# Kernel optimization log

Measured on AMD Instinct MI355X. Metric: run time of the kernel, lower is better.

Reference implementation:

```python
import jax, jax.numpy as jnp
import numpy as np

N_NODES = 50000
N_EDGES = 600000
IN_C, HID_C, OUT_C = 128, 128, 64
NUM_GRAPHS = 512


def sage_conv(x, src, dst, Wl, bl, Wr):
    """PyG SAGEConv (aggr='mean'): out = mean_{j->i} x_j @ Wl + bl + x_i @ Wr."""
    n = x.shape[0]
    msg = x[src]  # [E, d] gather
    agg = jax.ops.segment_sum(msg, dst, num_segments=n)
    deg = jax.ops.segment_sum(jnp.ones((src.shape[0], 1), x.dtype), dst, num_segments=n)
    agg = agg / jnp.maximum(deg, 1.0)
    return agg @ Wl + bl + x @ Wr


def setup_inputs() -> dict:
    key = jax.random.key(0)
    ks = jax.random.split(key, 12)
    x = jax.random.normal(ks[0], (N_NODES, IN_C), dtype=jnp.float32)
    edge_index = jax.random.randint(ks[1], (2, N_EDGES), 0, N_NODES, dtype=jnp.int32)
    cluster = jnp.sort(jax.random.randint(ks[2], (N_NODES,), 0, NUM_GRAPHS, dtype=jnp.int32))
    def lin(k, din, dout):
        s = 1.0 / np.sqrt(din)
        return (jax.random.uniform(k, (din, dout), jnp.float32, -s, s))
    return {
        "x": x, "edge_index": edge_index, "cluster": cluster,
        "Wl0": lin(ks[3], IN_C, HID_C), "bl0": jnp.zeros((HID_C,), jnp.float32), "Wr0": lin(ks[4], IN_C, HID_C),
        "Wl1": lin(ks[5], HID_C, HID_C), "bl1": jnp.zeros((HID_C,), jnp.float32), "Wr1": lin(ks[6], HID_C, HID_C),
        "Wl2": lin(ks[7], HID_C, OUT_C), "bl2": jnp.zeros((OUT_C,), jnp.float32), "Wr2": lin(ks[8], HID_C, OUT_C),
    }


def reference(x, edge_index, cluster, Wl0, bl0, Wr0, Wl1, bl1, Wr1, Wl2, bl2, Wr2):
    src, dst = edge_index[0], edge_index[1]
    out = None
    # hidden SAGEConv layers + relu (dropout inactive in eval)
    for Wl, bl, Wr in ((Wl0, bl0, Wr0), (Wl1, bl1, Wr1)):
        out = sage_conv(x, src, dst, Wl, bl, Wr)
        x = jax.nn.relu(out)
    # scatter-mean graph pooling over cluster ids
    gsum = jax.ops.segment_sum(x, cluster, num_segments=NUM_GRAPHS)
    gcnt = jax.ops.segment_sum(jnp.ones((x.shape[0], 1), x.dtype), cluster, num_segments=NUM_GRAPHS)
    g = gsum / jnp.maximum(gcnt, 1.0)
    # final conv + log-softmax over classes
    xf = sage_conv(x, src, dst, Wl2, bl2, Wr2)
    return (jax.nn.log_softmax(xf, axis=-1), out, g)
```

## Files before the change

### kernel.cpp

```cpp
#include <hip/hip_runtime.h>
#include <math.h>

#define NN 50000
#define NE 600000
#define NG 512

typedef unsigned int u32;
typedef unsigned short u16;

typedef __attribute__((ext_vector_type(8))) short bf16x8;
typedef __attribute__((ext_vector_type(4))) float f32x4;
typedef __attribute__((ext_vector_type(4))) unsigned int u32x4;

__device__ __forceinline__ float bf2f(u16 u) {
  return __uint_as_float(((u32)u) << 16);
}
__device__ __forceinline__ u16 f2bf(float f) {
  u32 u = __float_as_uint(f);
  u32 lsb = (u >> 16) & 1u;
  u += 0x7fffu + lsb;
  return (u16)(u >> 16);
}

__global__ __launch_bounds__(256)
void prep_k(const float* __restrict__ x, u32* __restrict__ xb,
            const int* __restrict__ ei, int* __restrict__ deg,
            const float* __restrict__ Wl0, const float* __restrict__ Wr0, u16* __restrict__ WbT0,
            const float* __restrict__ Wl1, const float* __restrict__ Wr1, u16* __restrict__ WbT1,
            const float* __restrict__ Wl2, u16* __restrict__ WlT2,
            const float* __restrict__ Wr2, u16* __restrict__ WrT2) {
  int b = blockIdx.x;
  int tid = threadIdx.x;
  if (b < 12500) {
    int t = b * 256 + tid;
    float2 v = ((const float2*)x)[t];
    xb[t] = (u32)f2bf(v.x) | ((u32)f2bf(v.y) << 16);
  } else if (b < 14844) {
    int e = (b - 12500) * 256 + tid;
    if (e < NE) atomicAdd(&deg[ei[NE + e]], 1);
  } else if (b < 15100) {
    bool w1 = (b >= 14972);
    int t = (b - (w1 ? 14972 : 14844)) * 256 + tid;
    int n = t >> 8;
    int k = t & 255;
    const float* Wl = w1 ? Wl1 : Wl0;
    const float* Wr = w1 ? Wr1 : Wr0;
    float v = (k < 128) ? Wl[k * 128 + n] : Wr[(k - 128) * 128 + n];
    int c = k >> 3, e = k & 7;
    u16* dst = w1 ? WbT1 : WbT0;
    dst[n * 256 + (((c ^ (n & 7)) << 3) | e)] = f2bf(v);
  } else {
    bool wr = (b >= 15132);
    int t = (b - (wr ? 15132 : 15100)) * 256 + tid;
    int n = t >> 7;
    int k = t & 127;
    const float* W = wr ? Wr2 : Wl2;
    float v = W[k * 64 + n];
    int c = k >> 3, e = k & 7;
    u16* dst = wr ? WrT2 : WlT2;
    dst[n * 128 + (((c ^ (n & 7)) << 3) | e)] = f2bf(v);
  }
}

__global__ __launch_bounds__(256)
void scan1_k(const int* __restrict__ deg, int* __restrict__ bsum) {
  __shared__ int s[256];
  int idx = blockIdx.x * 256 + threadIdx.x;
  int v = (idx < NN) ? deg[idx] : 0;
  s[threadIdx.x] = v;
  __syncthreads();
  for (int off = 128; off > 0; off >>= 1) {
    if (threadIdx.x < off) s[threadIdx.x] += s[threadIdx.x + off];
    __syncthreads();
  }
  if (threadIdx.x == 0) bsum[blockIdx.x] = s[0];
}

__global__ __launch_bounds__(256)
void scan2_k(const int* __restrict__ bsum, int* __restrict__ bofs, int* __restrict__ row_ptr) {
  __shared__ int s[256];
  int t = threadIdx.x;
  int v = (t < 196) ? bsum[t] : 0;
  s[t] = v;
  __syncthreads();
  for (int off = 1; off < 256; off <<= 1) {
    int add = (t >= off) ? s[t - off] : 0;
    __syncthreads();
    s[t] += add;
    __syncthreads();
  }
  if (t < 196) bofs[t] = s[t] - v;
  if (t == 0) row_ptr[NN] = NE;
}

__global__ __launch_bounds__(256)
void scan3_k(const int* __restrict__ deg, const int* __restrict__ bofs,
             int* __restrict__ row_ptr, int* __restrict__ cursor) {
  __shared__ int s[256];
  int idx = blockIdx.x * 256 + threadIdx.x;
  int t = threadIdx.x;
  int v = (idx < NN) ? deg[idx] : 0;
  s[t] = v;
  __syncthreads();
  for (int off = 1; off < 256; off <<= 1) {
    int add = (t >= off) ? s[t - off] : 0;
    __syncthreads();
    s[t] += add;
    __syncthreads();
  }
  if (idx < NN) {
    int p = bofs[blockIdx.x] + s[t] - v;
    row_ptr[idx] = p;
    cursor[idx] = p;
  }
}

__global__ __launch_bounds__(256)
void fill_k(const int* __restrict__ ei, int* __restrict__ cursor, int* __restrict__ perm) {
  int e = blockIdx.x * 256 + threadIdx.x;
  if (e >= NE) return;
  int pos = atomicAdd(&cursor[ei[NE + e]], 1);
  perm[pos] = ei[e];
}

__global__ __launch_bounds__(256)
void gather4_k(const u16* __restrict__ xb, const int* __restrict__ row_ptr,
               const int* __restrict__ perm, u16* __restrict__ aggb) {
  int wave = threadIdx.x >> 6;
  int lane = threadIdx.x & 63;
  int grp  = lane >> 4;
  int l16  = lane & 15;
  int n = (blockIdx.x * 4 + wave) * 4 + grp;
  int beg = row_ptr[n];
  int cnt = row_ptr[n + 1] - beg;
  int beg_s = min(beg, NE - 1);
  int last = max(cnt - 1, 0);
  int m = max(cnt, __shfl_xor(cnt, 16));
  int jmax = max(m, __shfl_xor(m, 32));
  float acc[8];
#pragma unroll
  for (int i = 0; i < 8; i++) acc[i] = 0.f;
  const u32x4* xv = (const u32x4*)xb;
  for (int base = 0; base < jmax; base += 8) {
    int idx[8];
#pragma unroll
    for (int j = 0; j < 8; j++) idx[j] = perm[beg_s + min(base + j, last)];
    u32x4 v[8];
#pragma unroll
    for (int j = 0; j < 8; j++) v[j] = xv[(size_t)idx[j] * 16 + l16];
#pragma unroll
    for (int j = 0; j < 8; j++) {
      bool live = (base + j) < cnt;
#pragma unroll
      for (int w = 0; w < 4; w++) {
        u32 u = v[j][w];
        acc[2 * w]     += live ? __uint_as_float(u << 16) : 0.f;
        acc[2 * w + 1] += live ? __uint_as_float(u & 0xffff0000u) : 0.f;
      }
    }
  }
  float inv = 1.0f / fmaxf((float)cnt, 1.0f);
  u32x4 o;
#pragma unroll
  for (int w = 0; w < 4; w++)
    o[w] = (u32)f2bf(acc[2 * w] * inv) | ((u32)f2bf(acc[2 * w + 1] * inv) << 16);
  ((u32x4*)aggb)[(size_t)n * 16 + l16] = o;
}

__global__ __launch_bounds__(256)
void gather8_k(const u16* __restrict__ yb, const int* __restrict__ row_ptr,
               const int* __restrict__ perm, u16* __restrict__ aggy) {
  int wave = threadIdx.x >> 6;
  int lane = threadIdx.x & 63;
  int grp  = lane >> 3;
  int li   = lane & 7;
  int n = (blockIdx.x * 4 + wave) * 8 + grp;
  int ns = min(n, NN - 1);
  int beg = row_ptr[ns];
  int cnt = row_ptr[ns + 1] - beg;
  int beg_s = min(beg, NE - 1);
  int last = max(cnt - 1, 0);
  int m = max(cnt, __shfl_xor(cnt, 8));
  m = max(m, __shfl_xor(m, 16));
  int jmax = max(m, __shfl_xor(m, 32));
  float acc[8];
#pragma unroll
  for (int i = 0; i < 8; i++) acc[i] = 0.f;
  const u32x4* xv = (const u32x4*)yb;
  for (int base = 0; base < jmax; base += 8) {
    int idx[8];
#pragma unroll
    for (int j = 0; j < 8; j++) idx[j] = perm[beg_s + min(base + j, last)];
    u32x4 v[8];
#pragma unroll
    for (int j = 0; j < 8; j++) v[j] = xv[(size_t)idx[j] * 8 + li];
#pragma unroll
    for (int j = 0; j < 8; j++) {
      bool live = (base + j) < cnt;
#pragma unroll
      for (int w = 0; w < 4; w++) {
        u32 u = v[j][w];
        acc[2 * w]     += live ? __uint_as_float(u << 16) : 0.f;
        acc[2 * w + 1] += live ? __uint_as_float(u & 0xffff0000u) : 0.f;
      }
    }
  }
  float inv = 1.0f / fmaxf((float)cnt, 1.0f);
  u32x4 o;
#pragma unroll
  for (int w = 0; w < 4; w++)
    o[w] = (u32)f2bf(acc[2 * w] * inv) | ((u32)f2bf(acc[2 * w + 1] * inv) << 16);
  if (n < NN) ((u32x4*)aggy)[(size_t)n * 8 + li] = o;
}

template<bool WRITE_PRE>
__global__ __launch_bounds__(256)
void sage_mfma_v2_k(const u16* __restrict__ aggb, const u16* __restrict__ xbin,
                    const u16* __restrict__ WbT, const float* __restrict__ bl,
                    u16* __restrict__ xb_out, float* __restrict__ out_pre) {
  __shared__ u16 wsh[128 * 256];
  int tid = threadIdx.x;
  {
    const u32x4* g = (const u32x4*)WbT;
    u32x4* l = (u32x4*)wsh;
#pragma unroll
    for (int i = 0; i < 16; i++)
      l[tid + i * 256] = g[tid + i * 256];
  }
  __syncthreads();

  int wave = tid >> 6;
  int lane = tid & 63;
  int quad = lane >> 4;
  int m16  = lane & 15;
  int r0 = blockIdx.x * 64 + wave * 16;

  int rowA = min(r0 + m16, NN - 1);
  const u16* pa = aggb + (size_t)rowA * 128 + quad * 8;
  const u16* px = xbin + (size_t)rowA * 128 + quad * 8;
  bf16x8 a[8];
#pragma unroll
  for (int j = 0; j < 4; j++) a[j]     = *(const bf16x8*)(pa + j * 32);
#pragma unroll
  for (int j = 0; j < 4; j++) a[4 + j] = *(const bf16x8*)(px + j * 32);

  f32x4 acc[8];
#pragma unroll
  for (int nt = 0; nt < 8; nt++) acc[nt] = (f32x4){0.f, 0.f, 0.f, 0.f};

  int swz = m16 & 7;
#pragma unroll
  for (int ks = 0; ks < 8; ks++) {
#pragma unroll
    for (int nt = 0; nt < 8; nt++) {
      const u16* bp = wsh + (nt * 16 + m16) * 256 + (((quad + ks * 4) ^ swz) << 3);
      bf16x8 b = *(const bf16x8*)bp;
      acc[nt] = __builtin_amdgcn_mfma_f32_16x16x32_bf16(a[ks], b, acc[nt], 0, 0, 0);
    }
  }

  float bv[8];
#pragma unroll
  for (int nt = 0; nt < 8; nt++) bv[nt] = bl[nt * 16 + m16];

  int rbase = r0 + quad * 4;
#pragma unroll
  for (int r = 0; r < 4; r++) {
    int row = rbase + r;
    if (row < NN) {
#pragma unroll
      for (int nt = 0; nt < 8; nt++) {
        int col = nt * 16 + m16;
        float v = acc[nt][r] + bv[nt];
        if (WRITE_PRE) out_pre[(size_t)row * 128 + col] = v;
        xb_out[(size_t)row * 128 + col] = f2bf(fmaxf(v, 0.f));
      }
    }
  }
}

__global__ __launch_bounds__(256)
void gemm64_k(const u16* __restrict__ xbin, const u16* __restrict__ WT,
              u16* __restrict__ yb) {
  __shared__ u16 wsh[64 * 128];
  int tid = threadIdx.x;
  {
    const u32x4* g = (const u32x4*)WT;
    u32x4* l = (u32x4*)wsh;
#pragma unroll
    for (int i = 0; i < 4; i++)
      l[tid + i * 256] = g[tid + i * 256];
  }
  __syncthreads();

  int wave = tid >> 6;
  int lane = tid & 63;
  int quad = lane >> 4;
  int m16  = lane & 15;
  int r0 = blockIdx.x * 64 + wave * 16;

  int rowA = min(r0 + m16, NN - 1);
  const u16* px = xbin + (size_t)rowA * 128 + quad * 8;
  bf16x8 a[4];
#pragma unroll
  for (int j = 0; j < 4; j++) a[j] = *(const bf16x8*)(px + j * 32);

  f32x4 acc[4];
#pragma unroll
  for (int nt = 0; nt < 4; nt++) acc[nt] = (f32x4){0.f, 0.f, 0.f, 0.f};

  int swz = m16 & 7;
#pragma unroll
  for (int ks = 0; ks < 4; ks++) {
#pragma unroll
    for (int nt = 0; nt < 4; nt++) {
      const u16* bp = wsh + (nt * 16 + m16) * 128 + (((ks * 4 + quad) ^ swz) << 3);
      bf16x8 b = *(const bf16x8*)bp;
      acc[nt] = __builtin_amdgcn_mfma_f32_16x16x32_bf16(a[ks], b, acc[nt], 0, 0, 0);
    }
  }

  int rbase = r0 + quad * 4;
#pragma unroll
  for (int r = 0; r < 4; r++) {
    int row = rbase + r;
    if (row < NN) {
#pragma unroll
      for (int nt = 0; nt < 4; nt++)
        yb[(size_t)row * 64 + nt * 16 + m16] = f2bf(acc[nt][r]);
    }
  }
}

__global__ __launch_bounds__(256)
void sage64f_k(const u16* __restrict__ aggy, const u16* __restrict__ xbin,
               const u16* __restrict__ WT, const float* __restrict__ bl,
               float* __restrict__ out) {
  __shared__ u16 wsh[64 * 128];
  int tid = threadIdx.x;
  {
    const u32x4* g = (const u32x4*)WT;
    u32x4* l = (u32x4*)wsh;
#pragma unroll
    for (int i = 0; i < 4; i++)
      l[tid + i * 256] = g[tid + i * 256];
  }
  __syncthreads();

  int wave = tid >> 6;
  int lane = tid & 63;
  int quad = lane >> 4;
  int m16  = lane & 15;
  int r0 = blockIdx.x * 64 + wave * 16;

  int rowA = min(r0 + m16, NN - 1);
  const u16* px = xbin + (size_t)rowA * 128 + quad * 8;
  bf16x8 a[4];
#pragma unroll
  for (int j = 0; j < 4; j++) a[j] = *(const bf16x8*)(px + j * 32);

  f32x4 acc[4];
#pragma unroll
  for (int nt = 0; nt < 4; nt++) acc[nt] = (f32x4){0.f, 0.f, 0.f, 0.f};

  int swz = m16 & 7;
#pragma unroll
  for (int ks = 0; ks < 4; ks++) {
#pragma unroll
    for (int nt = 0; nt < 4; nt++) {
      const u16* bp = wsh + (nt * 16 + m16) * 128 + (((ks * 4 + quad) ^ swz) << 3);
      bf16x8 b = *(const bf16x8*)bp;
      acc[nt] = __builtin_amdgcn_mfma_f32_16x16x32_bf16(a[ks], b, acc[nt], 0, 0, 0);
    }
  }

  float bv[4];
#pragma unroll
  for (int nt = 0; nt < 4; nt++) bv[nt] = bl[nt * 16 + m16];

  int rbase = r0 + quad * 4;
#pragma unroll
  for (int r = 0; r < 4; r++) {
    int row = rbase + r;
    int rs = min(row, NN - 1);
    float v0 = acc[0][r] + bv[0] + bf2f(aggy[(size_t)rs * 64 + m16]);
    float v1 = acc[1][r] + bv[1] + bf2f(aggy[(size_t)rs * 64 + 16 + m16]);
    float v2 = acc[2][r] + bv[2] + bf2f(aggy[(size_t)rs * 64 + 32 + m16]);
    float v3 = acc[3][r] + bv[3] + bf2f(aggy[(size_t)rs * 64 + 48 + m16]);
    float m = fmaxf(fmaxf(v0, v1), fmaxf(v2, v3));
#pragma unroll
    for (int mk = 1; mk <= 8; mk <<= 1) m = fmaxf(m, __shfl_xor(m, mk));
    float s = __expf(v0 - m) + __expf(v1 - m) + __expf(v2 - m) + __expf(v3 - m);
#pragma unroll
    for (int mk = 1; mk <= 8; mk <<= 1) s += __shfl_xor(s, mk);
    float ls = m + __logf(s);
    if (row < NN) {
      float* orow = out + (size_t)row * 64;
      orow[m16]      = v0 - ls;
      orow[16 + m16] = v1 - ls;
      orow[32 + m16] = v2 - ls;
      orow[48 + m16] = v3 - ls;
    }
  }
}

__global__ __launch_bounds__(256)
void pool_seg_k(const u16* __restrict__ xb, const int* __restrict__ cluster,
                float* __restrict__ g) {
  __shared__ float sh[256];
  int gid = blockIdx.x;
  int t = threadIdx.x;
  int ch = t & 127;
  int half = t >> 7;
  int lo = 0, hi = NN;
  while (lo < hi) { int mid = (lo + hi) >> 1; if (cluster[mid] < gid) lo = mid + 1; else hi = mid; }
  int beg = lo;
  hi = NN;
  while (lo < hi) { int mid = (lo + hi) >> 1; if (cluster[mid] < gid + 1) lo = mid + 1; else hi = mid; }
  int end = lo;
  float s0 = 0.f, s1 = 0.f;
  int n = beg + half;
  for (; n + 2 < end; n += 4) {
    s0 += bf2f(xb[(size_t)n * 128 + ch]);
    s1 += bf2f(xb[(size_t)(n + 2) * 128 + ch]);
  }
  if (n < end) s0 += bf2f(xb[(size_t)n * 128 + ch]);
  sh[t] = s0 + s1;
  __syncthreads();
  if (t < 128) {
    float s = sh[t] + sh[t + 128];
    g[gid * 128 + t] = s / fmaxf((float)(end - beg), 1.0f);
  }
}

extern "C" void kernel_launch(void* const* d_in, const int* in_sizes, int n_in,
                              void* d_out, int out_size, void* d_ws, size_t ws_size,
                              hipStream_t stream) {
  const float* x   = (const float*)d_in[0];
  const int*   ei  = (const int*)d_in[1];
  const int*   cl  = (const int*)d_in[2];
  const float* Wl0 = (const float*)d_in[3];
  const float* bl0 = (const float*)d_in[4];
  const float* Wr0 = (const float*)d_in[5];
  const float* Wl1 = (const float*)d_in[6];
  const float* bl1 = (const float*)d_in[7];
  const float* Wr1 = (const float*)d_in[8];
  const float* Wl2 = (const float*)d_in[9];
  const float* bl2 = (const float*)d_in[10];
  const float* Wr2 = (const float*)d_in[11];
  float* out = (float*)d_out;

  char* ws = (char*)d_ws;
  u16*   xb0     = (u16*)  (ws);
  u16*   xb1     = (u16*)  (ws + 12800000);
  u16*   xb2     = (u16*)  (ws + 25600000);
  u16*   aggb    = (u16*)  (ws + 38400000);
  u16*   y2      = aggb;
  u16*   aggy    = (u16*)  (ws + 38400000 + 6400000);
  u16*   WbT0    = (u16*)  (ws + 51200000);
  u16*   WbT1    = (u16*)  (ws + 51265536);
  u16*   WlT2    = (u16*)  (ws + 51331072);
  u16*   WrT2    = (u16*)  (ws + 51347456);
  int*   deg     = (int*)  (ws + 51363840);
  int*   row_ptr = (int*)  (ws + 51564032);
  int*   cursor  = (int*)  (ws + 51764736);
  int*   perm    = (int*)  (ws + 51964736);
  int*   bsum    = (int*)  (ws + 54364736);
  int*   bofs    = (int*)  (ws + 54365568);

  float* out_lsm = out;
  float* out_pre = out + 3200000;
  float* out_g   = out + 9600000;

  hipMemsetAsync(deg, 0, 200000, stream);
  prep_k<<<15164, 256, 0, stream>>>(x, (u32*)xb0, ei, deg,
                                    Wl0, Wr0, WbT0, Wl1, Wr1, WbT1,
                                    Wl2, WlT2, Wr2, WrT2);

  scan1_k<<<196, 256, 0, stream>>>(deg, bsum);
  scan2_k<<<1, 256, 0, stream>>>(bsum, bofs, row_ptr);
  scan3_k<<<196, 256, 0, stream>>>(deg, bofs, row_ptr, cursor);
  fill_k<<<2344, 256, 0, stream>>>(ei, cursor, perm);

  gather4_k<<<3125, 256, 0, stream>>>(xb0, row_ptr, perm, aggb);
  sage_mfma_v2_k<false><<<782, 256, 0, stream>>>(aggb, xb0, WbT0, bl0, xb1, nullptr);

  gather4_k<<<3125, 256, 0, stream>>>(xb1, row_ptr, perm, aggb);
  sage_mfma_v2_k<true><<<782, 256, 0, stream>>>(aggb, xb1, WbT1, bl1, xb2, out_pre);

  pool_seg_k<<<NG, 256, 0, stream>>>(xb2, cl, out_g);

  gemm64_k<<<782, 256, 0, stream>>>(xb2, WlT2, y2);
  gather8_k<<<1563, 256, 0, stream>>>(y2, row_ptr, perm, aggy);
  sage64f_k<<<782, 256, 0, stream>>>(aggy, xb2, WrT2, bl2, out_lsm);
}
```

Before: 281.7 us.

## Fuse neighbor-mean gather with SAGE GEMM and merge pooling with final-layer GEMM

Each hidden SAGE layer now runs as one kernel. A 16-node block gathers and averages neighbor features into LDS, then runs MFMA against the concatenated weights, read directly from global memory in an unswizzled layout. This removes the aggb round trip through memory and one launch per layer. Graph pooling and the 64-wide projection are merged into a single launch. The cost is that each block reloads the weight slice from global or L2 rather than staging it once in LDS, and the fused kernel pays a barrier between its gather and GEMM phases.

```diff
diff --git a/kernel.cpp b/kernel.cpp
--- a/kernel.cpp
+++ b/kernel.cpp
@@ -46,9 +46,8 @@
     const float* Wl = w1 ? Wl1 : Wl0;
     const float* Wr = w1 ? Wr1 : Wr0;
     float v = (k < 128) ? Wl[k * 128 + n] : Wr[(k - 128) * 128 + n];
-    int c = k >> 3, e = k & 7;
     u16* dst = w1 ? WbT1 : WbT0;
-    dst[n * 256 + (((c ^ (n & 7)) << 3) | e)] = f2bf(v);
+    dst[n * 256 + k] = f2bf(v);
   } else {
     bool wr = (b >= 15132);
     int t = (b - (wr ? 15132 : 15100)) * 256 + tid;
@@ -123,24 +122,31 @@
   perm[pos] = ei[e];
 }
 
-__global__ __launch_bounds__(256)
-void gather4_k(const u16* __restrict__ xb, const int* __restrict__ row_ptr,
-               const int* __restrict__ perm, u16* __restrict__ aggb) {
-  int wave = threadIdx.x >> 6;
-  int lane = threadIdx.x & 63;
+template<bool WRITE_PRE>
+__global__ __launch_bounds__(256)
+void sage_fused_k(const u16* __restrict__ xbin, const int* __restrict__ row_ptr,
+                  const int* __restrict__ perm, const u16* __restrict__ W,
+                  const float* __restrict__ bl,
+                  u16* __restrict__ xb_out, float* __restrict__ out_pre) {
+  __shared__ u16 ash[16 * 128];
+  int tid = threadIdx.x;
+  int wave = tid >> 6;
+  int lane = tid & 63;
   int grp  = lane >> 4;
   int l16  = lane & 15;
-  int n = (blockIdx.x * 4 + wave) * 4 + grp;
+
+  int rl = wave * 4 + grp;
+  int n = blockIdx.x * 16 + rl;
   int beg = row_ptr[n];
   int cnt = row_ptr[n + 1] - beg;
   int beg_s = min(beg, NE - 1);
   int last = max(cnt - 1, 0);
-  int m = max(cnt, __shfl_xor(cnt, 16));
-  int jmax = max(m, __shfl_xor(m, 32));
+  int mm = max(cnt, __shfl_xor(cnt, 16));
+  int jmax = max(mm, __shfl_xor(mm, 32));
   float acc[8];
 #pragma unroll
   for (int i = 0; i < 8; i++) acc[i] = 0.f;
-  const u32x4* xv = (const u32x4*)xb;
+  const u32x4* xv = (const u32x4*)xbin;
   for (int base = 0; base < jmax; base += 8) {
     int idx[8];
 #pragma unroll
@@ -159,12 +165,61 @@
       }
     }
   }
-  float inv = 1.0f / fmaxf((float)cnt, 1.0f);
-  u32x4 o;
-#pragma unroll
-  for (int w = 0; w < 4; w++)
-    o[w] = (u32)f2bf(acc[2 * w] * inv) | ((u32)f2bf(acc[2 * w + 1] * inv) << 16);
-  ((u32x4*)aggb)[(size_t)n * 16 + l16] = o;
+  {
+    float inv = 1.0f / fmaxf((float)cnt, 1.0f);
+    u32x4 o;
+#pragma unroll
+    for (int w = 0; w < 4; w++)
+      o[w] = (u32)f2bf(acc[2 * w] * inv) | ((u32)f2bf(acc[2 * w + 1] * inv) << 16);
+    ((u32x4*)ash)[rl * 16 + (l16 ^ (rl & 7))] = o;
+  }
+  __syncthreads();
+
+  int quad = grp;
+  int m16  = l16;
+  int c0 = wave * 32;
+  int r0 = blockIdx.x * 16;
+  int swz = m16 & 7;
+
+  bf16x8 a[8];
+#pragma unroll
+  for (int j = 0; j < 4; j++)
+    a[j] = *(const bf16x8*)(ash + m16 * 128 + (((j * 4 + quad) ^ swz) << 3));
+  {
+    const u16* px = xbin + (size_t)(r0 + m16) * 128 + quad * 8;
+#pragma unroll
+    for (int j = 0; j < 4; j++)
+      a[4 + j] = *(const bf16x8*)(px + j * 32);
+  }
+
+  f32x4 acc2[2];
+  acc2[0] = (f32x4){0.f, 0.f, 0.f, 0.f};
+  acc2[1] = (f32x4){0.f, 0.f, 0.f, 0.f};
+  const u16* brow0 = W + (size_t)(c0 + m16) * 256 + quad * 8;
+  const u16* brow1 = W + (size_t)(c0 + 16 + m16) * 256 + quad * 8;
+#pragma unroll
+  for (int ks = 0; ks < 8; ks++) {
+    bf16x8 b0 = *(const bf16x8*)(brow0 + ks * 32);
+    bf16x8 b1 = *(const bf16x8*)(brow1 + ks * 32);
+    acc2[0] = __builtin_amdgcn_mfma_f32_16x16x32_bf16(a[ks], b0, acc2[0], 0, 0, 0);
+    acc2[1] = __builtin_amdgcn_mfma_f32_16x16x32_bf16(a[ks], b1, acc2[1], 0, 0, 0);
+  }
+
+  float bv0 = bl[c0 + m16];
+  float bv1 = bl[c0 + 16 + m16];
+  int rbase = r0 + quad * 4;
+#pragma unroll
+  for (int r = 0; r < 4; r++) {
+    int row = rbase + r;
+    float v0 = acc2[0][r] + bv0;
+    float v1 = acc2[1][r] + bv1;
+    if (WRITE_PRE) {
+      out_pre[(size_t)row * 128 + c0 + m16]      = v0;
+      out_pre[(size_t)row * 128 + c0 + 16 + m16] = v1;
+    }
+    xb_out[(size_t)row * 128 + c0 + m16]      = f2bf(fmaxf(v0, 0.f));
+    xb_out[(size_t)row * 128 + c0 + 16 + m16] = f2bf(fmaxf(v1, 0.f));
+  }
 }
 
 __global__ __launch_bounds__(256)
@@ -213,19 +268,45 @@
   if (n < NN) ((u32x4*)aggy)[(size_t)n * 8 + li] = o;
 }
 
-template<bool WRITE_PRE>
-__global__ __launch_bounds__(256)
-void sage_mfma_v2_k(const u16* __restrict__ aggb, const u16* __restrict__ xbin,
-                    const u16* __restrict__ WbT, const float* __restrict__ bl,
-                    u16* __restrict__ xb_out, float* __restrict__ out_pre) {
-  __shared__ u16 wsh[128 * 256];
+__global__ __launch_bounds__(256)
+void post_k(const u16* __restrict__ xb2, const int* __restrict__ cluster,
+            float* __restrict__ g, const u16* __restrict__ WlT2,
+            u16* __restrict__ yb) {
+  __shared__ u16 wsh[64 * 128];
   int tid = threadIdx.x;
+  if (blockIdx.x < NG) {
+    float* sh = (float*)wsh;
+    int gid = blockIdx.x;
+    int ch = tid & 127;
+    int half = tid >> 7;
+    int lo = 0, hi = NN;
+    while (lo < hi) { int mid = (lo + hi) >> 1; if (cluster[mid] < gid) lo = mid + 1; else hi = mid; }
+    int beg = lo;
+    hi = NN;
+    while (lo < hi) { int mid = (lo + hi) >> 1; if (cluster[mid] < gid + 1) lo = mid + 1; else hi = mid; }
+    int end = lo;
+    float s0 = 0.f, s1 = 0.f;
+    int n = beg + half;
+    for (; n + 2 < end; n += 4) {
+      s0 += bf2f(xb2[(size_t)n * 128 + ch]);
+      s1 += bf2f(xb2[(size_t)(n + 2) * 128 + ch]);
+    }
+    if (n < end) s0 += bf2f(xb2[(size_t)n * 128 + ch]);
+    sh[tid] = s0 + s1;
+    __syncthreads();
+    if (tid < 128) {
+      float s = sh[tid] + sh[tid + 128];
+      g[gid * 128 + tid] = s / fmaxf((float)(end - beg), 1.0f);
+    }
+    return;
+  }
+  int bid = blockIdx.x - NG;
   {
-    const u32x4* g = (const u32x4*)WbT;
+    const u32x4* gw = (const u32x4*)WlT2;
     u32x4* l = (u32x4*)wsh;
 #pragma unroll
-    for (int i = 0; i < 16; i++)
-      l[tid + i * 256] = g[tid + i * 256];
+    for (int i = 0; i < 4; i++)
+      l[tid + i * 256] = gw[tid + i * 256];
   }
   __syncthreads();
 
@@ -233,74 +314,10 @@
   int lane = tid & 63;
   int quad = lane >> 4;
   int m16  = lane & 15;
-  int r0 = blockIdx.x * 64 + wave * 16;
+  int r0 = bid * 64 + wave * 16;
 
   int rowA = min(r0 + m16, NN - 1);
-  const u16* pa = aggb + (size_t)rowA * 128 + quad * 8;
-  const u16* px = xbin + (size_t)rowA * 128 + quad * 8;
-  bf16x8 a[8];
-#pragma unroll
-  for (int j = 0; j < 4; j++) a[j]     = *(const bf16x8*)(pa + j * 32);
-#pragma unroll
-  for (int j = 0; j < 4; j++) a[4 + j] = *(const bf16x8*)(px + j * 32);
-
-  f32x4 acc[8];
-#pragma unroll
-  for (int nt = 0; nt < 8; nt++) acc[nt] = (f32x4){0.f, 0.f, 0.f, 0.f};
-
-  int swz = m16 & 7;
-#pragma unroll
-  for (int ks = 0; ks < 8; ks++) {
-#pragma unroll
-    for (int nt = 0; nt < 8; nt++) {
-      const u16* bp = wsh + (nt * 16 + m16) * 256 + (((quad + ks * 4) ^ swz) << 3);
-      bf16x8 b = *(const bf16x8*)bp;
-      acc[nt] = __builtin_amdgcn_mfma_f32_16x16x32_bf16(a[ks], b, acc[nt], 0, 0, 0);
-    }
-  }
-
-  float bv[8];
-#pragma unroll
-  for (int nt = 0; nt < 8; nt++) bv[nt] = bl[nt * 16 + m16];
-
-  int rbase = r0 + quad * 4;
-#pragma unroll
-  for (int r = 0; r < 4; r++) {
-    int row = rbase + r;
-    if (row < NN) {
-#pragma unroll
-      for (int nt = 0; nt < 8; nt++) {
-        int col = nt * 16 + m16;
-        float v = acc[nt][r] + bv[nt];
-        if (WRITE_PRE) out_pre[(size_t)row * 128 + col] = v;
-        xb_out[(size_t)row * 128 + col] = f2bf(fmaxf(v, 0.f));
-      }
-    }
-  }
-}
-
-__global__ __launch_bounds__(256)
-void gemm64_k(const u16* __restrict__ xbin, const u16* __restrict__ WT,
-              u16* __restrict__ yb) {
-  __shared__ u16 wsh[64 * 128];
-  int tid = threadIdx.x;
-  {
-    const u32x4* g = (const u32x4*)WT;
-    u32x4* l = (u32x4*)wsh;
-#pragma unroll
-    for (int i = 0; i < 4; i++)
-      l[tid + i * 256] = g[tid + i * 256];
-  }
-  __syncthreads();
-
-  int wave = tid >> 6;
-  int lane = tid & 63;
-  int quad = lane >> 4;
-  int m16  = lane & 15;
-  int r0 = blockIdx.x * 64 + wave * 16;
-
-  int rowA = min(r0 + m16, NN - 1);
-  const u16* px = xbin + (size_t)rowA * 128 + quad * 8;
+  const u16* px = xb2 + (size_t)rowA * 128 + quad * 8;
   bf16x8 a[4];
 #pragma unroll
   for (int j = 0; j < 4; j++) a[j] = *(const bf16x8*)(px + j * 32);
@@ -401,35 +418,6 @@
       orow[32 + m16] = v2 - ls;
       orow[48 + m16] = v3 - ls;
     }
-  }
-}
-
-__global__ __launch_bounds__(256)
-void pool_seg_k(const u16* __restrict__ xb, const int* __restrict__ cluster,
-                float* __restrict__ g) {
-  __shared__ float sh[256];
-  int gid = blockIdx.x;
-  int t = threadIdx.x;
-  int ch = t & 127;
-  int half = t >> 7;
-  int lo = 0, hi = NN;
-  while (lo < hi) { int mid = (lo + hi) >> 1; if (cluster[mid] < gid) lo = mid + 1; else hi = mid; }
-  int beg = lo;
-  hi = NN;
-  while (lo < hi) { int mid = (lo + hi) >> 1; if (cluster[mid] < gid + 1) lo = mid + 1; else hi = mid; }
-  int end = lo;
-  float s0 = 0.f, s1 = 0.f;
-  int n = beg + half;
-  for (; n + 2 < end; n += 4) {
-    s0 += bf2f(xb[(size_t)n * 128 + ch]);
-    s1 += bf2f(xb[(size_t)(n + 2) * 128 + ch]);
-  }
-  if (n < end) s0 += bf2f(xb[(size_t)n * 128 + ch]);
-  sh[t] = s0 + s1;
-  __syncthreads();
-  if (t < 128) {
-    float s = sh[t] + sh[t + 128];
-    g[gid * 128 + t] = s / fmaxf((float)(end - beg), 1.0f);
   }
 }
 
@@ -454,9 +442,8 @@
   u16*   xb0     = (u16*)  (ws);
   u16*   xb1     = (u16*)  (ws + 12800000);
   u16*   xb2     = (u16*)  (ws + 25600000);
-  u16*   aggb    = (u16*)  (ws + 38400000);
-  u16*   y2      = aggb;
-  u16*   aggy    = (u16*)  (ws + 38400000 + 6400000);
+  u16*   y2      = (u16*)  (ws + 38400000);
+  u16*   aggy    = (u16*)  (ws + 44800000);
   u16*   WbT0    = (u16*)  (ws + 51200000);
   u16*   WbT1    = (u16*)  (ws + 51265536);
   u16*   WlT2    = (u16*)  (ws + 51331072);
@@ -482,15 +469,12 @@
   scan3_k<<<196, 256, 0, stream>>>(deg, bofs, row_ptr, cursor);
   fill_k<<<2344, 256, 0, stream>>>(ei, cursor, perm);
 
-  gather4_k<<<3125, 256, 0, stream>>>(xb0, row_ptr, perm, aggb);
-  sage_mfma_v2_k<false><<<782, 256, 0, stream>>>(aggb, xb0, WbT0, bl0, xb1, nullptr);
-
-  gather4_k<<<3125, 256, 0, stream>>>(xb1, row_ptr, perm, aggb);
-  sage_mfma_v2_k<true><<<782, 256, 0, stream>>>(aggb, xb1, WbT1, bl1, xb2, out_pre);
-
-  pool_seg_k<<<NG, 256, 0, stream>>>(xb2, cl, out_g);
-
-  gemm64_k<<<782, 256, 0, stream>>>(xb2, WlT2, y2);
+  sage_fused_k<false><<<3125, 256, 0, stream>>>(xb0, row_ptr, perm, WbT0, bl0, xb1, nullptr);
+
+  sage_fused_k<true><<<3125, 256, 0, stream>>>(xb1, row_ptr, perm, WbT1, bl1, xb2, out_pre);
+
+  post_k<<<NG + 782, 256, 0, stream>>>(xb2, cl, out_g, WlT2, y2);
+
   gather8_k<<<1563, 256, 0, stream>>>(y2, row_ptr, perm, aggy);
   sage64f_k<<<782, 256, 0, stream>>>(aggy, xb2, WrT2, bl2, out_lsm);
 }
```

New measurement: 302.9 us. +7.5%, slower.

## Fuse CSR build and tail kernels into persistent kernels with grid barriers

Applied to the files above, without the earlier changes.

Merges the three scan kernels and the fill kernel into one 196-block kernel that uses software grid barriers in place of launch boundaries. The separate pool, gemm64, gather8 and final sage64 kernels become a single 1024-block persistent kernel that also synchronises through atomic grid barriers. The aim is to remove several kernel launches and their inter-kernel gaps. In exchange it depends on every block being co-resident, or the spin barriers deadlock, and the fill phase now runs on fewer blocks.

```diff
diff --git a/kernel.cpp b/kernel.cpp
--- a/kernel.cpp
+++ b/kernel.cpp
@@ -20,6 +20,17 @@
   u32 lsb = (u >> 16) & 1u;
   u += 0x7fffu + lsb;
   return (u16)(u >> 16);
+}
+
+__device__ __forceinline__ void gridbar(int* bar, int nblk) {
+  __syncthreads();
+  if (threadIdx.x == 0) {
+    __threadfence();
+    atomicAdd(bar, 1);
+    while (atomicAdd(bar, 0) < nblk) __builtin_amdgcn_s_sleep(8);
+    __threadfence();
+  }
+  __syncthreads();
 }
 
 __global__ __launch_bounds__(256)
@@ -63,24 +74,33 @@
 }
 
 __global__ __launch_bounds__(256)
-void scan1_k(const int* __restrict__ deg, int* __restrict__ bsum) {
-  __shared__ int s[256];
-  int idx = blockIdx.x * 256 + threadIdx.x;
-  int v = (idx < NN) ? deg[idx] : 0;
-  s[threadIdx.x] = v;
-  __syncthreads();
-  for (int off = 128; off > 0; off >>= 1) {
-    if (threadIdx.x < off) s[threadIdx.x] += s[threadIdx.x + off];
-    __syncthreads();
-  }
-  if (threadIdx.x == 0) bsum[blockIdx.x] = s[0];
-}
-
-__global__ __launch_bounds__(256)
-void scan2_k(const int* __restrict__ bsum, int* __restrict__ bofs, int* __restrict__ row_ptr) {
+void csr_k(const int* __restrict__ ei, const int* __restrict__ deg,
+           int* __restrict__ bsum, int* __restrict__ row_ptr,
+           int* __restrict__ cursor, int* __restrict__ perm, int* __restrict__ bars) {
   __shared__ int s[256];
   int t = threadIdx.x;
-  int v = (t < 196) ? bsum[t] : 0;
+  int b = blockIdx.x;
+  int idx = b * 256 + t;
+  int v = (idx < NN) ? deg[idx] : 0;
+
+  s[t] = v;
+  __syncthreads();
+  for (int off = 128; off > 0; off >>= 1) {
+    if (t < off) s[t] += s[t + off];
+    __syncthreads();
+  }
+  if (t == 0) bsum[b] = s[0];
+  gridbar(&bars[0], 196);
+
+  s[t] = (t < b) ? bsum[t] : 0;
+  __syncthreads();
+  for (int off = 128; off > 0; off >>= 1) {
+    if (t < off) s[t] += s[t + off];
+    __syncthreads();
+  }
+  int bofs_b = s[0];
+  __syncthreads();
+
   s[t] = v;
   __syncthreads();
   for (int off = 1; off < 256; off <<= 1) {
@@ -89,38 +109,18 @@
     s[t] += add;
     __syncthreads();
   }
-  if (t < 196) bofs[t] = s[t] - v;
-  if (t == 0) row_ptr[NN] = NE;
-}
-
-__global__ __launch_bounds__(256)
-void scan3_k(const int* __restrict__ deg, const int* __restrict__ bofs,
-             int* __restrict__ row_ptr, int* __restrict__ cursor) {
-  __shared__ int s[256];
-  int idx = blockIdx.x * 256 + threadIdx.x;
-  int t = threadIdx.x;
-  int v = (idx < NN) ? deg[idx] : 0;
-  s[t] = v;
-  __syncthreads();
-  for (int off = 1; off < 256; off <<= 1) {
-    int add = (t >= off) ? s[t - off] : 0;
-    __syncthreads();
-    s[t] += add;
-    __syncthreads();
-  }
   if (idx < NN) {
-    int p = bofs[blockIdx.x] + s[t] - v;
+    int p = bofs_b + s[t] - v;
     row_ptr[idx] = p;
     cursor[idx] = p;
   }
-}
-
-__global__ __launch_bounds__(256)
-void fill_k(const int* __restrict__ ei, int* __restrict__ cursor, int* __restrict__ perm) {
-  int e = blockIdx.x * 256 + threadIdx.x;
-  if (e >= NE) return;
-  int pos = atomicAdd(&cursor[ei[NE + e]], 1);
-  perm[pos] = ei[e];
+  if (b == 0 && t == 0) row_ptr[NN] = NE;
+  gridbar(&bars[1], 196);
+
+  for (int e = b * 256 + t; e < NE; e += 196 * 256) {
+    int pos = atomicAdd(&cursor[ei[NE + e]], 1);
+    perm[pos] = ei[e];
+  }
 }
 
 __global__ __launch_bounds__(256)
@@ -167,52 +167,6 @@
   ((u32x4*)aggb)[(size_t)n * 16 + l16] = o;
 }
 
-__global__ __launch_bounds__(256)
-void gather8_k(const u16* __restrict__ yb, const int* __restrict__ row_ptr,
-               const int* __restrict__ perm, u16* __restrict__ aggy) {
-  int wave = threadIdx.x >> 6;
-  int lane = threadIdx.x & 63;
-  int grp  = lane >> 3;
-  int li   = lane & 7;
-  int n = (blockIdx.x * 4 + wave) * 8 + grp;
-  int ns = min(n, NN - 1);
-  int beg = row_ptr[ns];
-  int cnt = row_ptr[ns + 1] - beg;
-  int beg_s = min(beg, NE - 1);
-  int last = max(cnt - 1, 0);
-  int m = max(cnt, __shfl_xor(cnt, 8));
-  m = max(m, __shfl_xor(m, 16));
-  int jmax = max(m, __shfl_xor(m, 32));
-  float acc[8];
-#pragma unroll
-  for (int i = 0; i < 8; i++) acc[i] = 0.f;
-  const u32x4* xv = (const u32x4*)yb;
-  for (int base = 0; base < jmax; base += 8) {
-    int idx[8];
-#pragma unroll
-    for (int j = 0; j < 8; j++) idx[j] = perm[beg_s + min(base + j, last)];
-    u32x4 v[8];
-#pragma unroll
-    for (int j = 0; j < 8; j++) v[j] = xv[(size_t)idx[j] * 8 + li];
-#pragma unroll
-    for (int j = 0; j < 8; j++) {
-      bool live = (base + j) < cnt;
-#pragma unroll
-      for (int w = 0; w < 4; w++) {
-        u32 u = v[j][w];
-        acc[2 * w]     += live ? __uint_as_float(u << 16) : 0.f;
-        acc[2 * w + 1] += live ? __uint_as_float(u & 0xffff0000u) : 0.f;
-      }
-    }
-  }
-  float inv = 1.0f / fmaxf((float)cnt, 1.0f);
-  u32x4 o;
-#pragma unroll
-  for (int w = 0; w < 4; w++)
-    o[w] = (u32)f2bf(acc[2 * w] * inv) | ((u32)f2bf(acc[2 * w + 1] * inv) << 16);
-  if (n < NN) ((u32x4*)aggy)[(size_t)n * 8 + li] = o;
-}
-
 template<bool WRITE_PRE>
 __global__ __launch_bounds__(256)
 void sage_mfma_v2_k(const u16* __restrict__ aggb, const u16* __restrict__ xbin,
@@ -279,157 +233,210 @@
   }
 }
 
-__global__ __launch_bounds__(256)
-void gemm64_k(const u16* __restrict__ xbin, const u16* __restrict__ WT,
-              u16* __restrict__ yb) {
+__global__ __launch_bounds__(256, 4)
+void tail_k(const u16* __restrict__ xb2, const int* __restrict__ cluster,
+            float* __restrict__ g, const u16* __restrict__ WlT2,
+            u16* __restrict__ y2, const int* __restrict__ row_ptr,
+            const int* __restrict__ perm, u16* __restrict__ aggy,
+            const u16* __restrict__ WrT2, const float* __restrict__ bl2,
+            float* __restrict__ out, int* __restrict__ bars) {
   __shared__ u16 wsh[64 * 128];
   int tid = threadIdx.x;
-  {
-    const u32x4* g = (const u32x4*)WT;
-    u32x4* l = (u32x4*)wsh;
-#pragma unroll
-    for (int i = 0; i < 4; i++)
-      l[tid + i * 256] = g[tid + i * 256];
-  }
-  __syncthreads();
-
   int wave = tid >> 6;
   int lane = tid & 63;
   int quad = lane >> 4;
   int m16  = lane & 15;
-  int r0 = blockIdx.x * 64 + wave * 16;
-
-  int rowA = min(r0 + m16, NN - 1);
-  const u16* px = xbin + (size_t)rowA * 128 + quad * 8;
-  bf16x8 a[4];
-#pragma unroll
-  for (int j = 0; j < 4; j++) a[j] = *(const bf16x8*)(px + j * 32);
-
-  f32x4 acc[4];
-#pragma unroll
-  for (int nt = 0; nt < 4; nt++) acc[nt] = (f32x4){0.f, 0.f, 0.f, 0.f};
-
   int swz = m16 & 7;
-#pragma unroll
-  for (int ks = 0; ks < 4; ks++) {
-#pragma unroll
-    for (int nt = 0; nt < 4; nt++) {
-      const u16* bp = wsh + (nt * 16 + m16) * 128 + (((ks * 4 + quad) ^ swz) << 3);
-      bf16x8 b = *(const bf16x8*)bp;
-      acc[nt] = __builtin_amdgcn_mfma_f32_16x16x32_bf16(a[ks], b, acc[nt], 0, 0, 0);
-    }
-  }
-
-  int rbase = r0 + quad * 4;
-#pragma unroll
-  for (int r = 0; r < 4; r++) {
-    int row = rbase + r;
-    if (row < NN) {
-#pragma unroll
-      for (int nt = 0; nt < 4; nt++)
-        yb[(size_t)row * 64 + nt * 16 + m16] = f2bf(acc[nt][r]);
-    }
-  }
-}
-
-__global__ __launch_bounds__(256)
-void sage64f_k(const u16* __restrict__ aggy, const u16* __restrict__ xbin,
-               const u16* __restrict__ WT, const float* __restrict__ bl,
-               float* __restrict__ out) {
-  __shared__ u16 wsh[64 * 128];
-  int tid = threadIdx.x;
+
+  int wb = blockIdx.x;
+  if (wb < 782) {
+    const u32x4* gw = (const u32x4*)WlT2;
+    u32x4* l = (u32x4*)wsh;
+#pragma unroll
+    for (int i = 0; i < 4; i++) l[tid + i * 256] = gw[tid + i * 256];
+    __syncthreads();
+    int r0 = wb * 64 + wave * 16;
+    int rowA = min(r0 + m16, NN - 1);
+    const u16* px = xb2 + (size_t)rowA * 128 + quad * 8;
+    bf16x8 a[4];
+#pragma unroll
+    for (int j = 0; j < 4; j++) a[j] = *(const bf16x8*)(px + j * 32);
+    f32x4 acc[4];
+#pragma unroll
+    for (int nt = 0; nt < 4; nt++) acc[nt] = (f32x4){0.f, 0.f, 0.f, 0.f};
+#pragma unroll
+    for (int ks = 0; ks < 4; ks++) {
+#pragma unroll
+      for (int nt = 0; nt < 4; nt++) {
+        const u16* bp = wsh + (nt * 16 + m16) * 128 + (((ks * 4 + quad) ^ swz) << 3);
+        bf16x8 b = *(const bf16x8*)bp;
+        acc[nt] = __builtin_amdgcn_mfma_f32_16x16x32_bf16(a[ks], b, acc[nt], 0, 0, 0);
+      }
+    }
+    int rbase = r0 + quad * 4;
+#pragma unroll
+    for (int r = 0; r < 4; r++) {
+      int row = rbase + r;
+      if (row < NN) {
+#pragma unroll
+        for (int nt = 0; nt < 4; nt++)
+          y2[(size_t)row * 64 + nt * 16 + m16] = f2bf(acc[nt][r]);
+      }
+    }
+  } else if (wb < 1294) {
+    float* shf = (float*)wsh;
+    int gid = wb - 782;
+    int ch = tid & 127;
+    int half = tid >> 7;
+    int lo = 0, hi = NN;
+    while (lo < hi) { int mid = (lo + hi) >> 1; if (cluster[mid] < gid) lo = mid + 1; else hi = mid; }
+    int beg = lo;
+    hi = NN;
+    while (lo < hi) { int mid = (lo + hi) >> 1; if (cluster[mid] < gid + 1) lo = mid + 1; else hi = mid; }
+    int end = lo;
+    float s0 = 0.f, s1 = 0.f;
+    int n = beg + half;
+    for (; n + 2 < end; n += 4) {
+      s0 += bf2f(xb2[(size_t)n * 128 + ch]);
+      s1 += bf2f(xb2[(size_t)(n + 2) * 128 + ch]);
+    }
+    if (n < end) s0 += bf2f(xb2[(size_t)n * 128 + ch]);
+    __syncthreads();
+    shf[tid] = s0 + s1;
+    __syncthreads();
+    if (tid < 128) {
+      float s = shf[tid] + shf[tid + 128];
+      g[gid * 128 + tid] = s / fmaxf((float)(end - beg), 1.0f);
+    }
+  }
   {
-    const u32x4* g = (const u32x4*)WT;
+    int wb2 = blockIdx.x + 1024;
+    if (wb2 < 1294) {
+      float* shf = (float*)wsh;
+      int gid = wb2 - 782;
+      int ch = tid & 127;
+      int half = tid >> 7;
+      int lo = 0, hi = NN;
+      while (lo < hi) { int mid = (lo + hi) >> 1; if (cluster[mid] < gid) lo = mid + 1; else hi = mid; }
+      int beg = lo;
+      hi = NN;
+      while (lo < hi) { int mid = (lo + hi) >> 1; if (cluster[mid] < gid + 1) lo = mid + 1; else hi = mid; }
+      int end = lo;
+      float s0 = 0.f, s1 = 0.f;
+      int n = beg + half;
+      for (; n + 2 < end; n += 4) {
+        s0 += bf2f(xb2[(size_t)n * 128 + ch]);
+        s1 += bf2f(xb2[(size_t)(n + 2) * 128 + ch]);
+      }
+      if (n < end) s0 += bf2f(xb2[(size_t)n * 128 + ch]);
+      __syncthreads();
+      shf[tid] = s0 + s1;
+      __syncthreads();
+      if (tid < 128) {
+        float s = shf[tid] + shf[tid + 128];
+        g[gid * 128 + tid] = s / fmaxf((float)(end - beg), 1.0f);
+      }
+    }
+  }
+  gridbar(&bars[2], 1024);
+
+  for (int it = 0; it < 2; it++) {
+    int vb = blockIdx.x + it * 1024;
+    if (vb >= 1563) break;
+    int grp8 = lane >> 3;
+    int li   = lane & 7;
+    int n = (vb * 4 + wave) * 8 + grp8;
+    int ns = min(n, NN - 1);
+    int beg = row_ptr[ns];
+    int cnt = row_ptr[ns + 1] - beg;
+    int beg_s = min(beg, NE - 1);
+    int last = max(cnt - 1, 0);
+    int m = max(cnt, __shfl_xor(cnt, 8));
+    m = max(m, __shfl_xor(m, 16));
+    int jmax = max(m, __shfl_xor(m, 32));
+    float acc[8];
+#pragma unroll
+    for (int i = 0; i < 8; i++) acc[i] = 0.f;
+    const u32x4* xv = (const u32x4*)y2;
+    for (int base = 0; base < jmax; base += 8) {
+      int idx[8];
+#pragma unroll
+      for (int j = 0; j < 8; j++) idx[j] = perm[beg_s + min(base + j, last)];
+      u32x4 v[8];
+#pragma unroll
+      for (int j = 0; j < 8; j++) v[j] = xv[(size_t)idx[j] * 8 + li];
+#pragma unroll
+      for (int j = 0; j < 8; j++) {
+        bool live = (base + j) < cnt;
+#pragma unroll
+        for (int w = 0; w < 4; w++) {
+          u32 u = v[j][w];
+          acc[2 * w]     += live ? __uint_as_float(u << 16) : 0.f;
+          acc[2 * w + 1] += live ? __uint_as_float(u & 0xffff0000u) : 0.f;
+        }
+      }
+    }
+    float inv = 1.0f / fmaxf((float)cnt, 1.0f);
+    u32x4 o;
+#pragma unroll
+    for (int w = 0; w < 4; w++)
+      o[w] = (u32)f2bf(acc[2 * w] * inv) | ((u32)f2bf(acc[2 * w + 1] * inv) << 16);
+    if (n < NN) ((u32x4*)aggy)[(size_t)n * 8 + li] = o;
+  }
+  gridbar(&bars[3], 1024);
+
+  if (blockIdx.x < 782) {
+    const u32x4* gw = (const u32x4*)WrT2;
     u32x4* l = (u32x4*)wsh;
 #pragma unroll
-    for (int i = 0; i < 4; i++)
-      l[tid + i * 256] = g[tid + i * 256];
-  }
-  __syncthreads();
-
-  int wave = tid >> 6;
-  int lane = tid & 63;
-  int quad = lane >> 4;
-  int m16  = lane & 15;
-  int r0 = blockIdx.x * 64 + wave * 16;
-
-  int rowA = min(r0 + m16, NN - 1);
-  const u16* px = xbin + (size_t)rowA * 128 + quad * 8;
-  bf16x8 a[4];
-#pragma unroll
-  for (int j = 0; j < 4; j++) a[j] = *(const bf16x8*)(px + j * 32);
-
-  f32x4 acc[4];
-#pragma unroll
-  for (int nt = 0; nt < 4; nt++) acc[nt] = (f32x4){0.f, 0.f, 0.f, 0.f};
-
-  int swz = m16 & 7;
-#pragma unroll
-  for (int ks = 0; ks < 4; ks++) {
-#pragma unroll
-    for (int nt = 0; nt < 4; nt++) {
-      const u16* bp = wsh + (nt * 16 + m16) * 128 + (((ks * 4 + quad) ^ swz) << 3);
-      bf16x8 b = *(const bf16x8*)bp;
-      acc[nt] = __builtin_amdgcn_mfma_f32_16x16x32_bf16(a[ks], b, acc[nt], 0, 0, 0);
-    }
-  }
-
-  float bv[4];
-#pragma unroll
-  for (int nt = 0; nt < 4; nt++) bv[nt] = bl[nt * 16 + m16];
-
-  int rbase = r0 + quad * 4;
-#pragma unroll
-  for (int r = 0; r < 4; r++) {
-    int row = rbase + r;
-    int rs = min(row, NN - 1);
-    float v0 = acc[0][r] + bv[0] + bf2f(aggy[(size_t)rs * 64 + m16]);
-    float v1 = acc[1][r] + bv[1] + bf2f(aggy[(size_t)rs * 64 + 16 + m16]);
-    float v2 = acc[2][r] + bv[2] + bf2f(aggy[(size_t)rs * 64 + 32 + m16]);
-    float v3 = acc[3][r] + bv[3] + bf2f(aggy[(size_t)rs * 64 + 48 + m16]);
-    float m = fmaxf(fmaxf(v0, v1), fmaxf(v2, v3));
-#pragma unroll
-    for (int mk = 1; mk <= 8; mk <<= 1) m = fmaxf(m, __shfl_xor(m, mk));
-    float s = __expf(v0 - m) + __expf(v1 - m) + __expf(v2 - m) + __expf(v3 - m);
-#pragma unroll
-    for (int mk = 1; mk <= 8; mk <<= 1) s += __shfl_xor(s, mk);
-    float ls = m + __logf(s);
-    if (row < NN) {
-      float* orow = out + (size_t)row * 64;
-      orow[m16]      = v0 - ls;
-      orow[16 + m16] = v1 - ls;
-      orow[32 + m16] = v2 - ls;
-      orow[48 + m16] = v3 - ls;
-    }
-  }
-}
-
-__global__ __launch_bounds__(256)
-void pool_seg_k(const u16* __restrict__ xb, const int* __restrict__ cluster,
-                float* __restrict__ g) {
-  __shared__ float sh[256];
-  int gid = blockIdx.x;
-  int t = threadIdx.x;
-  int ch = t & 127;
-  int half = t >> 7;
-  int lo = 0, hi = NN;
-  while (lo < hi) { int mid = (lo + hi) >> 1; if (cluster[mid] < gid) lo = mid + 1; else hi = mid; }
-  int beg = lo;
-  hi = NN;
-  while (lo < hi) { int mid = (lo + hi) >> 1; if (cluster[mid] < gid + 1) lo = mid + 1; else hi = mid; }
-  int end = lo;
-  float s0 = 0.f, s1 = 0.f;
-  int n = beg + half;
-  for (; n + 2 < end; n += 4) {
-    s0 += bf2f(xb[(size_t)n * 128 + ch]);
-    s1 += bf2f(xb[(size_t)(n + 2) * 128 + ch]);
-  }
-  if (n < end) s0 += bf2f(xb[(size_t)n * 128 + ch]);
-  sh[t] = s0 + s1;
-  __syncthreads();
-  if (t < 128) {
-    float s = sh[t] + sh[t + 128];
-    g[gid * 128 + t] = s / fmaxf((float)(end - beg), 1.0f);
+    for (int i = 0; i < 4; i++) l[tid + i * 256] = gw[tid + i * 256];
+    __syncthreads();
+
+    int r0 = blockIdx.x * 64 + wave * 16;
+    int rowA = min(r0 + m16, NN - 1);
+    const u16* px = xb2 + (size_t)rowA * 128 + quad * 8;
+    bf16x8 a[4];
+#pragma unroll
+    for (int j = 0; j < 4; j++) a[j] = *(const bf16x8*)(px + j * 32);
+    f32x4 acc[4];
+#pragma unroll
+    for (int nt = 0; nt < 4; nt++) acc[nt] = (f32x4){0.f, 0.f, 0.f, 0.f};
+#pragma unroll
+    for (int ks = 0; ks < 4; ks++) {
+#pragma unroll
+      for (int nt = 0; nt < 4; nt++) {
+        const u16* bp = wsh + (nt * 16 + m16) * 128 + (((ks * 4 + quad) ^ swz) << 3);
+        bf16x8 b = *(const bf16x8*)bp;
+        acc[nt] = __builtin_amdgcn_mfma_f32_16x16x32_bf16(a[ks], b, acc[nt], 0, 0, 0);
+      }
+    }
+    float bv[4];
+#pragma unroll
+    for (int nt = 0; nt < 4; nt++) bv[nt] = bl2[nt * 16 + m16];
+    int rbase = r0 + quad * 4;
+#pragma unroll
+    for (int r = 0; r < 4; r++) {
+      int row = rbase + r;
+      int rs = min(row, NN - 1);
+      float v0 = acc[0][r] + bv[0] + bf2f(aggy[(size_t)rs * 64 + m16]);
+      float v1 = acc[1][r] + bv[1] + bf2f(aggy[(size_t)rs * 64 + 16 + m16]);
+      float v2 = acc[2][r] + bv[2] + bf2f(aggy[(size_t)rs * 64 + 32 + m16]);
+      float v3 = acc[3][r] + bv[3] + bf2f(aggy[(size_t)rs * 64 + 48 + m16]);
+      float m = fmaxf(fmaxf(v0, v1), fmaxf(v2, v3));
+#pragma unroll
+      for (int mk = 1; mk <= 8; mk <<= 1) m = fmaxf(m, __shfl_xor(m, mk));
+      float s = __expf(v0 - m) + __expf(v1 - m) + __expf(v2 - m) + __expf(v3 - m);
+#pragma unroll
+      for (int mk = 1; mk <= 8; mk <<= 1) s += __shfl_xor(s, mk);
+      float ls = m + __logf(s);
+      if (row < NN) {
+        float* orow = out + (size_t)row * 64;
+        orow[m16]      = v0 - ls;
+        orow[16 + m16] = v1 - ls;
+        orow[32 + m16] = v2 - ls;
+        orow[48 + m16] = v3 - ls;
+      }
+    }
   }
 }
 
@@ -456,31 +463,29 @@
   u16*   xb2     = (u16*)  (ws + 25600000);
   u16*   aggb    = (u16*)  (ws + 38400000);
   u16*   y2      = aggb;
-  u16*   aggy    = (u16*)  (ws + 38400000 + 6400000);
+  u16*   aggy    = (u16*)  (ws + 44800000);
   u16*   WbT0    = (u16*)  (ws + 51200000);
   u16*   WbT1    = (u16*)  (ws + 51265536);
   u16*   WlT2    = (u16*)  (ws + 51331072);
   u16*   WrT2    = (u16*)  (ws + 51347456);
   int*   deg     = (int*)  (ws + 51363840);
+  int*   bars    = (int*)  (ws + 51563840);
   int*   row_ptr = (int*)  (ws + 51564032);
   int*   cursor  = (int*)  (ws + 51764736);
   int*   perm    = (int*)  (ws + 51964736);
   int*   bsum    = (int*)  (ws + 54364736);
-  int*   bofs    = (int*)  (ws + 54365568);
 
   float* out_lsm = out;
   float* out_pre = out + 3200000;
   float* out_g   = out + 9600000;
 
-  hipMemsetAsync(deg, 0, 200000, stream);
+  hipMemsetAsync(deg, 0, 200016, stream);
+
   prep_k<<<15164, 256, 0, stream>>>(x, (u32*)xb0, ei, deg,
                                     Wl0, Wr0, WbT0, Wl1, Wr1, WbT1,
                                     Wl2, WlT2, Wr2, WrT2);
 
-  scan1_k<<<196, 256, 0, stream>>>(deg, bsum);
-  scan2_k<<<1, 256, 0, stream>>>(bsum, bofs, row_ptr);
-  scan3_k<<<196, 256, 0, stream>>>(deg, bofs, row_ptr, cursor);
-  fill_k<<<2344, 256, 0, stream>>>(ei, cursor, perm);
+  csr_k<<<196, 256, 0, stream>>>(ei, deg, bsum, row_ptr, cursor, perm, bars);
 
   gather4_k<<<3125, 256, 0, stream>>>(xb0, row_ptr, perm, aggb);
   sage_mfma_v2_k<false><<<782, 256, 0, stream>>>(aggb, xb0, WbT0, bl0, xb1, nullptr);
@@ -488,9 +493,6 @@
   gather4_k<<<3125, 256, 0, stream>>>(xb1, row_ptr, perm, aggb);
   sage_mfma_v2_k<true><<<782, 256, 0, stream>>>(aggb, xb1, WbT1, bl1, xb2, out_pre);
 
-  pool_seg_k<<<NG, 256, 0, stream>>>(xb2, cl, out_g);
-
-  gemm64_k<<<782, 256, 0, stream>>>(xb2, WlT2, y2);
-  gather8_k<<<1563, 256, 0, stream>>>(y2, row_ptr, perm, aggy);
-  sage64f_k<<<782, 256, 0, stream>>>(aggy, xb2, WrT2, bl2, out_lsm);
-}
+  tail_k<<<1024, 256, 0, stream>>>(xb2, cl, out_g, WlT2, y2, row_ptr, perm,
+                                   aggy, WrT2, bl2, out_lsm, bars);
+}
```

Result: slower. 531.7 us (+88.7%).
